# Kernel optimization log

Measured on AMD Instinct MI355X. Metric: run time of the kernel, lower is better.

The kernel has to match this reference:

```python
import jax, jax.numpy as jnp
import numpy as np
from jax import lax

B, T, H = 2, 1024, 768
E = 64          # num_experts (global pool)
I = 256         # moe_intermediate_size
TOP_K = 8       # num_experts_per_tok


def setup_inputs() -> dict:
    key = jax.random.key(0)
    k0, k1, k2, k3, k4 = jax.random.split(key, 5)
    hidden_states = jax.random.normal(k0, (B, T, H), dtype=jnp.float32)
    router_w = jax.random.normal(k1, (E, H), dtype=jnp.float32) * 0.02
    w_gate = jax.random.normal(k2, (E, H, I), dtype=jnp.float32) * 0.02
    w_up = jax.random.normal(k3, (E, H, I), dtype=jnp.float32) * 0.02
    w_down = jax.random.normal(k4, (E, I, H), dtype=jnp.float32) * 0.02
    return {"hidden_states": hidden_states, "router_w": router_w,
            "w_gate": w_gate, "w_up": w_up, "w_down": w_down}


def reference(hidden_states, router_w, w_gate, w_up, w_down):
    b, t, h = hidden_states.shape
    x = hidden_states.reshape(-1, h)                      # [N, H]
    n = x.shape[0]
    # --- Qwen3MoeTopKRouter: softmax -> top-k -> renormalize ---
    logits = x @ router_w.T                               # [N, E]
    probs = jax.nn.softmax(logits.astype(jnp.float32), axis=-1)
    top_w, top_i = lax.top_k(probs, TOP_K)                # [N, K]
    top_w = top_w / jnp.sum(top_w, axis=-1, keepdims=True)  # norm_topk_prob
    top_w = top_w.astype(x.dtype)
    # dense routing-weight matrix [N, E]; zero for unselected experts
    rw = jnp.zeros((n, E), dtype=x.dtype).at[
        jnp.arange(n)[:, None], top_i].set(top_w)
    # --- Qwen3MoeExperts: per-expert SwiGLU, combined by routing weights ---
    def step(acc, inp):
        wg, wu, wd, w = inp                               # wg/wu [H,I], wd [I,H], w [N]
        hmid = jax.nn.silu(x @ wg) * (x @ wu)             # [N, I]
        return acc + w[:, None] * (hmid @ wd), None
    out, _ = lax.scan(step, jnp.zeros_like(x),
                      (w_gate, w_up, w_down, rw.T))
    return out.reshape(b, t, h)
```

## Files before the change

kernel.cpp:

```cpp
#include <hip/hip_runtime.h>
#include <hip/hip_bf16.h>
#include <math.h>

#define N_TOK 2048
#define H_DIM 768
#define E_NUM 64
#define I_DIM 256
#define TOPK 8
#define NPAIR (N_TOK * TOPK)

typedef __attribute__((ext_vector_type(8))) short short8;
typedef __attribute__((ext_vector_type(4))) short short4v;
typedef __attribute__((ext_vector_type(4))) float f32x4;

__device__ inline ushort f2bf(float f) {
  unsigned u = __builtin_bit_cast(unsigned, f);
  u += 0x7fffu + ((u >> 16) & 1u);
  return (ushort)(u >> 16);
}

__device__ inline float bf2f(ushort h) {
  return __builtin_bit_cast(float, (unsigned)h << 16);
}

__device__ inline unsigned pack2(float a, float b) {
  return (unsigned)f2bf(a) | ((unsigned)f2bf(b) << 16);
}

__device__ inline f32x4 mfma16(short8 a, short8 b, f32x4 c) {
  return __builtin_amdgcn_mfma_f32_16x16x32_bf16(a, b, c, 0, 0, 0);
}

__device__ __forceinline__ void gload_lds16(const ushort* g, ushort* l) {
  __builtin_amdgcn_global_load_lds(
      (const __attribute__((address_space(1))) unsigned int*)g,
      (__attribute__((address_space(3))) unsigned int*)l, 16, 0, 0);
}

#define RT_KC 256
__global__ __launch_bounds__(256) void router_gemm(const float* __restrict__ x,
                                                   const float* __restrict__ rw,
                                                   float* __restrict__ part,
                                                   ushort* __restrict__ xbf) {
  const int t0 = blockIdx.x * 64, k0 = blockIdx.y * RT_KC;
  __shared__ float xs[64][68];
  __shared__ float ws[64][68];
  const int tid = threadIdx.x;
  const int tx = tid & 15, ty = tid >> 4;
  float acc[4][4] = {};
  for (int kc = 0; kc < RT_KC; kc += 64) {
    __syncthreads();
    {
      const int r = tid >> 2, q = tid & 3;
      const float4* srcx = (const float4*)&x[(size_t)(t0 + r) * H_DIM + k0 + kc];
      const float4* srcw = (const float4*)&rw[(size_t)r * H_DIM + k0 + kc];
      float4* dstx = (float4*)&xs[r][0];
      float4* dstw = (float4*)&ws[r][0];
      ushort* xb = xbf + (size_t)(t0 + r) * H_DIM + k0 + kc + q * 16;
      #pragma unroll
      for (int j = 0; j < 4; ++j) {
        float4 vx = srcx[q * 4 + j];
        dstx[q * 4 + j] = vx;
        dstw[q * 4 + j] = srcw[q * 4 + j];
        uint2 b;
        b.x = pack2(vx.x, vx.y);
        b.y = pack2(vx.z, vx.w);
        *(uint2*)(xb + j * 4) = b;
      }
    }
    __syncthreads();
    #pragma unroll
    for (int k4 = 0; k4 < 16; ++k4) {
      float4 a0 = *(float4*)&xs[ty * 4 + 0][k4 * 4];
      float4 a1 = *(float4*)&xs[ty * 4 + 1][k4 * 4];
      float4 a2 = *(float4*)&xs[ty * 4 + 2][k4 * 4];
      float4 a3 = *(float4*)&xs[ty * 4 + 3][k4 * 4];
      float4 b0 = *(float4*)&ws[tx * 4 + 0][k4 * 4];
      float4 b1 = *(float4*)&ws[tx * 4 + 1][k4 * 4];
      float4 b2 = *(float4*)&ws[tx * 4 + 2][k4 * 4];
      float4 b3 = *(float4*)&ws[tx * 4 + 3][k4 * 4];
      #define RFMA(i, j, av, bv) \
        acc[i][j] = fmaf(av.x, bv.x, fmaf(av.y, bv.y, fmaf(av.z, bv.z, fmaf(av.w, bv.w, acc[i][j]))))
      RFMA(0, 0, a0, b0); RFMA(0, 1, a0, b1); RFMA(0, 2, a0, b2); RFMA(0, 3, a0, b3);
      RFMA(1, 0, a1, b0); RFMA(1, 1, a1, b1); RFMA(1, 2, a1, b2); RFMA(1, 3, a1, b3);
      RFMA(2, 0, a2, b0); RFMA(2, 1, a2, b1); RFMA(2, 2, a2, b2); RFMA(2, 3, a2, b3);
      RFMA(3, 0, a3, b0); RFMA(3, 1, a3, b1); RFMA(3, 2, a3, b2); RFMA(3, 3, a3, b3);
      #undef RFMA
    }
  }
  float* pp = part + ((size_t)blockIdx.y * N_TOK + t0) * E_NUM;
  #pragma unroll
  for (int i = 0; i < 4; ++i)
    #pragma unroll
    for (int j = 0; j < 4; ++j)
      pp[(ty * 4 + i) * E_NUM + tx * 4 + j] = acc[i][j];
}

__global__ __launch_bounds__(256) void router_topk(const float* __restrict__ part,
                                                   int* __restrict__ topi,
                                                   float* __restrict__ topw) {
  const int t = blockIdx.x * 4 + (threadIdx.x >> 6);
  const int l = threadIdx.x & 63;
  float myv = part[(size_t)t * E_NUM + l] +
              part[((size_t)N_TOK + t) * E_NUM + l] +
              part[((size_t)2 * N_TOK + t) * E_NUM + l];
  float topv[TOPK]; int topx[TOPK];
  #pragma unroll
  for (int k = 0; k < TOPK; ++k) {
    float bv = myv; int bi = l;
    #pragma unroll
    for (int off = 32; off > 0; off >>= 1) {
      float ov = __shfl_xor(bv, off, 64);
      int oi = __shfl_xor(bi, off, 64);
      if (ov > bv || (ov == bv && oi < bi)) { bv = ov; bi = oi; }
    }
    topv[k] = bv; topx[k] = bi;
    if (l == bi) myv = -INFINITY;
  }
  if (l == 0) {
    float mx = topv[0], w[TOPK], s = 0.f;
    #pragma unroll
    for (int k = 0; k < TOPK; ++k) { w[k] = __expf(topv[k] - mx); s += w[k]; }
    float inv = 1.f / s;
    #pragma unroll
    for (int k = 0; k < TOPK; ++k) {
      topi[t * TOPK + k] = topx[k];
      topw[t * TOPK + k] = w[k] * inv;
    }
  }
}

__global__ __launch_bounds__(256) void scatter64(const int* __restrict__ topi,
                                                 int* __restrict__ offsets,
                                                 int* __restrict__ toklist,
                                                 int* __restrict__ pairpos) {
  const int e = blockIdx.x;
  const int tid = threadIdx.x, l = tid & 63, w = tid >> 6;
  __shared__ int h[E_NUM];
  __shared__ int wcnt[4];
  __shared__ int sbase;
  if (tid < E_NUM) h[tid] = 0;
  __syncthreads();
  int cnt = 0;
  for (int c = 0; c < NPAIR / 4; c += 64) {
    const int idx = w * (NPAIR / 4) + c + l;
    const int ei = topi[idx];
    atomicAdd(&h[ei], 1);
    cnt += __popcll(__ballot(ei == e));
  }
  if (l == 0) wcnt[w] = cnt;
  __syncthreads();
  if (tid == 0) {
    int s = 0;
    for (int ee = 0; ee < e; ++ee) s += h[ee];
    sbase = s;
    offsets[e] = s;
    if (e == E_NUM - 1) offsets[E_NUM] = s + h[e];
  }
  __syncthreads();
  int base = sbase;
  for (int ww = 0; ww < 4; ++ww)
    if (ww < w) base += wcnt[ww];
  for (int c = 0; c < NPAIR / 4; c += 64) {
    const int idx = w * (NPAIR / 4) + c + l;
    const bool p = (topi[idx] == e);
    const unsigned long long m = __ballot(p);
    if (p) {
      const int pos = base + __popcll(m & ((1ull << l) - 1ull));
      toklist[pos] = idx >> 3;
      pairpos[idx] = pos;
    }
    base += __popcll(m);
  }
}

#define K1_TB 192
#define KC1 64
#define NCH1 12
#define BS_ST 74
__global__ __launch_bounds__(512, 4) void k1_gateup(const ushort* __restrict__ xbf,
                                                    const float* __restrict__ wg,
                                                    const float* __restrict__ wu,
                                                    const int* __restrict__ offsets,
                                                    const int* __restrict__ toklist,
                                                    ushort* __restrict__ hmid) {
  const int e = blockIdx.y, ib = blockIdx.x;
  const int i0 = ib * 64;
  const int start = offsets[e], cnt = offsets[e + 1] - start;
  const int tokbase = blockIdx.z * K1_TB;
  if (tokbase >= cnt) return;
  const int cntb = min(K1_TB, cnt - tokbase);

  __shared__ __align__(16) ushort xs[2][K1_TB][64];
  __shared__ __align__(16) ushort Bs[128][BS_ST];
  __shared__ int tks[K1_TB];

  const int tid = threadIdx.x;
  if (tid < K1_TB) tks[tid] = toklist[start + tokbase + min(tid, cntb - 1)];
  __syncthreads();

  const int l = tid & 63, wid = tid >> 6;
  const int tf = wid & 3, icw = wid >> 2;
  const int la15 = l & 15;
  const int lxor = (l & 7) ^ ((l >> 3) & 7);

  const ushort* srcx0 = xbf + (size_t)tks[24 * wid + 0 + (l >> 3)] * H_DIM + lxor * 8;
  const ushort* srcx1 = xbf + (size_t)tks[24 * wid + 8 + (l >> 3)] * H_DIM + lxor * 8;
  const ushort* srcx2 = xbf + (size_t)tks[24 * wid + 16 + (l >> 3)] * H_DIM + lxor * 8;

  const int q = tid & 15, kp = tid >> 4;
  const float* wgp = wg + (size_t)e * H_DIM * I_DIM + i0 + 4 * q;
  const float* wup = wu + (size_t)e * H_DIM * I_DIM + i0 + 4 * q;

  f32x4 accg[3][2] = {};
  f32x4 accu[3][2] = {};
  const int ko = (l >> 4) * 8;

  float4 g0 = *(const float4*)(wgp + (size_t)(2 * kp) * I_DIM);
  float4 g1 = *(const float4*)(wgp + (size_t)(2 * kp + 1) * I_DIM);
  float4 u0 = *(const float4*)(wup + (size_t)(2 * kp) * I_DIM);
  float4 u1 = *(const float4*)(wup + (size_t)(2 * kp + 1) * I_DIM);
  gload_lds16(srcx0, &xs[0][24 * wid + 0][0]);
  gload_lds16(srcx1, &xs[0][24 * wid + 8][0]);
  gload_lds16(srcx2, &xs[0][24 * wid + 16][0]);

  for (int n = 0; n < NCH1; ++n) {
    const int cur = n & 1, nxt = cur ^ 1;
    *(unsigned*)&Bs[q * 4 + 0][2 * kp] = pack2(g0.x, g1.x);
    *(unsigned*)&Bs[q * 4 + 1][2 * kp] = pack2(g0.y, g1.y);
    *(unsigned*)&Bs[q * 4 + 2][2 * kp] = pack2(g0.z, g1.z);
    *(unsigned*)&Bs[q * 4 + 3][2 * kp] = pack2(g0.w, g1.w);
    *(unsigned*)&Bs[64 + q * 4 + 0][2 * kp] = pack2(u0.x, u1.x);
    *(unsigned*)&Bs[64 + q * 4 + 1][2 * kp] = pack2(u0.y, u1.y);
    *(unsigned*)&Bs[64 + q * 4 + 2][2 * kp] = pack2(u0.z, u1.z);
    *(unsigned*)&Bs[64 + q * 4 + 3][2 * kp] = pack2(u0.w, u1.w);
    if (n + 1 < NCH1) {
      const int kh = (n + 1) * KC1;
      g0 = *(const float4*)(wgp + (size_t)(kh + 2 * kp) * I_DIM);
      g1 = *(const float4*)(wgp + (size_t)(kh + 2 * kp + 1) * I_DIM);
      u0 = *(const float4*)(wup + (size_t)(kh + 2 * kp) * I_DIM);
      u1 = *(const float4*)(wup + (size_t)(kh + 2 * kp + 1) * I_DIM);
      gload_lds16(srcx0 + kh, &xs[nxt][24 * wid + 0][0]);
      gload_lds16(srcx1 + kh, &xs[nxt][24 * wid + 8][0]);
      gload_lds16(srcx2 + kh, &xs[nxt][24 * wid + 16][0]);
      asm volatile("s_waitcnt vmcnt(7) lgkmcnt(0)" ::: "memory");
      __builtin_amdgcn_sched_barrier(0);
      __builtin_amdgcn_s_barrier();
    } else {
      asm volatile("s_waitcnt vmcnt(0) lgkmcnt(0)" ::: "memory");
      __builtin_amdgcn_sched_barrier(0);
      __builtin_amdgcn_s_barrier();
    }
    #pragma unroll
    for (int ks = 0; ks < 2; ++ks) {
      const int kof = ks * 32 + ko;
      const int sg8 = ((ks * 4 + (l >> 4)) ^ (l & 7)) * 8;
      short8 bg0 = *(const short8*)&Bs[icw * 32 + la15][kof];
      short8 bg1 = *(const short8*)&Bs[icw * 32 + 16 + la15][kof];
      short8 bu0 = *(const short8*)&Bs[64 + icw * 32 + la15][kof];
      short8 bu1 = *(const short8*)&Bs[64 + icw * 32 + 16 + la15][kof];
      __builtin_amdgcn_s_setprio(1);
      #pragma unroll
      for (int rf = 0; rf < 3; ++rf) {
        short8 a = *(const short8*)&xs[cur][tf * 48 + rf * 16 + la15][sg8];
        accg[rf][0] = mfma16(a, bg0, accg[rf][0]);
        accg[rf][1] = mfma16(a, bg1, accg[rf][1]);
        accu[rf][0] = mfma16(a, bu0, accu[rf][0]);
        accu[rf][1] = mfma16(a, bu1, accu[rf][1]);
      }
      __builtin_amdgcn_s_setprio(0);
    }
    asm volatile("s_waitcnt lgkmcnt(0)" ::: "memory");
    __builtin_amdgcn_sched_barrier(0);
    __builtin_amdgcn_s_barrier();
  }

  ushort* tbuf = &xs[0][0][0];
  #pragma unroll
  for (int rf = 0; rf < 3; ++rf)
    #pragma unroll
    for (int c = 0; c < 2; ++c)
      #pragma unroll
      for (int jj = 0; jj < 4; ++jj) {
        const int row = tf * 48 + rf * 16 + (l >> 4) * 4 + jj;
        const int col = icw * 32 + c * 16 + la15;
        float g = accg[rf][c][jj];
        float hm = g / (1.f + __expf(-g)) * accu[rf][c][jj];
        tbuf[row * 72 + col] = f2bf(hm);
      }
  __syncthreads();
  #pragma unroll
  for (int p = 0; p < 2; ++p) {
    const int row = (tid >> 2) + p * 128, cs = tid & 3;
    if (row < cntb) {
      short8 v0 = *(const short8*)&tbuf[row * 72 + cs * 16];
      short8 v1 = *(const short8*)&tbuf[row * 72 + cs * 16 + 8];
      ushort* dst = hmid + (size_t)(start + tokbase + row) * I_DIM + i0 + cs * 16;
      *(short8*)dst = v0;
      *(short8*)(dst + 8) = v1;
    }
  }
}

#define K2_TB 256
#define KC2 128
#define DS_ST 138
__global__ __launch_bounds__(512) void k2_down(const ushort* __restrict__ hmid,
                                               const float* __restrict__ wd,
                                               const int* __restrict__ offsets,
                                               ushort* __restrict__ out_pairs) {
  const int e = blockIdx.y, hs = blockIdx.x;
  const int h0 = hs * 192;
  const int start = offsets[e], cnt = offsets[e + 1] - start;
  const int tokbase = blockIdx.z * K2_TB;
  if (tokbase >= cnt) return;
  const int tm = min(K2_TB, cnt - tokbase);

  __shared__ ushort Ds[192][DS_ST];

  const int tid = threadIdx.x, l = tid & 63, wid = tid >> 6;
  const int tf = wid & 3, ch = wid >> 2;
  const int la15 = l & 15;
  const int ko = (l >> 4) * 8;
  f32x4 acc[4][6] = {};

  int p[4];
  #pragma unroll
  for (int rf = 0; rf < 4; ++rf)
    p[rf] = min(start + tokbase + tf * 64 + rf * 16 + la15, NPAIR - 1);

  const float* wde = wd + (size_t)e * I_DIM * H_DIM;

  for (int kh = 0; kh < I_DIM; kh += KC2) {
    __syncthreads();
    #pragma unroll
    for (int it = 0; it < 6; ++it) {
      int idx = tid + it * 512;
      int qq = idx % 48, m = idx / 48;
      const int k0 = 2 * m;
      const float* src = wde + (size_t)(kh + k0) * H_DIM + h0 + qq * 4;
      float4 v0 = *(const float4*)src;
      float4 v1 = *(const float4*)(src + H_DIM);
      *(unsigned*)&Ds[qq * 4 + 0][k0] = pack2(v0.x, v1.x);
      *(unsigned*)&Ds[qq * 4 + 1][k0] = pack2(v0.y, v1.y);
      *(unsigned*)&Ds[qq * 4 + 2][k0] = pack2(v0.z, v1.z);
      *(unsigned*)&Ds[qq * 4 + 3][k0] = pack2(v0.w, v1.w);
    }
    __syncthreads();
    #pragma unroll
    for (int ks = 0; ks < 4; ++ks) {
      const int kof = ks * 32 + ko;
      short8 a[4];
      #pragma unroll
      for (int rf = 0; rf < 4; ++rf)
        a[rf] = *(const short8*)(hmid + (size_t)p[rf] * I_DIM + kh + kof);
      __builtin_amdgcn_s_setprio(1);
      #pragma unroll
      for (int cf = 0; cf < 6; ++cf) {
        short8 b = *(const short8*)&Ds[ch * 96 + cf * 16 + la15][kof];
        #pragma unroll
        for (int rf = 0; rf < 4; ++rf)
          acc[rf][cf] = mfma16(a[rf], b, acc[rf][cf]);
      }
      __builtin_amdgcn_s_setprio(0);
    }
  }

  const int rgrp = l >> 4;
  #pragma unroll
  for (int rf = 0; rf < 4; ++rf)
    #pragma unroll
    for (int jj = 0; jj < 4; ++jj) {
      int r = tf * 64 + rf * 16 + rgrp * 4 + jj;
      if (r < tm) {
        const size_t prow = (size_t)(start + tokbase + r);
        #pragma unroll
        for (int cf = 0; cf < 6; ++cf) {
          int hcol = h0 + ch * 96 + cf * 16 + la15;
          out_pairs[prow * H_DIM + hcol] = f2bf(acc[rf][cf][jj]);
        }
      }
    }
}

__global__ __launch_bounds__(192) void moe_reduce(const ushort* __restrict__ out_pairs,
                                                  const int* __restrict__ pairpos,
                                                  const float* __restrict__ topw,
                                                  float* __restrict__ out) {
  const int t = blockIdx.x;
  const int c = threadIdx.x;
  float4 acc = make_float4(0.f, 0.f, 0.f, 0.f);
  #pragma unroll
  for (int k = 0; k < TOPK; ++k) {
    const int pos = pairpos[t * TOPK + k];
    const float w = topw[t * TOPK + k];
    short4v v = *(const short4v*)&out_pairs[(size_t)pos * H_DIM + c * 4];
    acc.x = fmaf(w, bf2f((ushort)v[0]), acc.x);
    acc.y = fmaf(w, bf2f((ushort)v[1]), acc.y);
    acc.z = fmaf(w, bf2f((ushort)v[2]), acc.z);
    acc.w = fmaf(w, bf2f((ushort)v[3]), acc.w);
  }
  *(float4*)&out[(size_t)t * H_DIM + c * 4] = acc;
}

extern "C" void kernel_launch(void* const* d_in, const int* in_sizes, int n_in,
                              void* d_out, int out_size, void* d_ws, size_t ws_size,
                              hipStream_t stream) {
  const float* x  = (const float*)d_in[0];
  const float* rw = (const float*)d_in[1];
  const float* wg = (const float*)d_in[2];
  const float* wu = (const float*)d_in[3];
  const float* wd = (const float*)d_in[4];
  float* out = (float*)d_out;

  char* ws = (char*)d_ws;
  int*    topi     = (int*)(ws + 0);
  float*  topw     = (float*)(ws + 65536);
  int*    offsets  = (int*)(ws + 131072);
  int*    toklist  = (int*)(ws + 132608);
  int*    pairpos  = (int*)(ws + 264192);
  ushort* xbf      = (ushort*)(ws + 331776);
  ushort* hmid     = (ushort*)(ws + 3477504);
  float*  rpart    = (float*)(ws + 3477504);
  ushort* out_pairs= (ushort*)(ws + 11866112);

  router_gemm<<<dim3(N_TOK / 64, 3), 256, 0, stream>>>(x, rw, rpart, xbf);
  router_topk<<<N_TOK / 4, 256, 0, stream>>>(rpart, topi, topw);
  scatter64<<<E_NUM, 256, 0, stream>>>(topi, offsets, toklist, pairpos);
  k1_gateup<<<dim3(4, E_NUM, 11), 512, 0, stream>>>(xbf, wg, wu, offsets, toklist, hmid);
  k2_down<<<dim3(4, E_NUM, 8), 512, 0, stream>>>(hmid, wd, offsets, out_pairs);
  moe_reduce<<<N_TOK, 192, 0, stream>>>(out_pairs, pairpos, topw, out);
}
```

Baseline: 127.3 us.

## Fuse router GEMM and top-k selection into a single kernel

Merges the split-K router GEMM and the separate top-k kernel into one kernel. Each block computes full-K logits for 64 tokens, stages them in shared memory, and runs wave-level top-k with renormalised softmax weights. This removes a kernel launch and the global partial-logit round trip. It reduces the grid from 96 to 32 blocks and serialises the full 768-deep reduction per block, which lowers parallelism.

```diff
diff --git a/kernel.cpp b/kernel.cpp
--- a/kernel.cpp
+++ b/kernel.cpp
@@ -37,26 +37,26 @@
       (__attribute__((address_space(3))) unsigned int*)l, 16, 0, 0);
 }
 
-#define RT_KC 256
-__global__ __launch_bounds__(256) void router_gemm(const float* __restrict__ x,
-                                                   const float* __restrict__ rw,
-                                                   float* __restrict__ part,
-                                                   ushort* __restrict__ xbf) {
-  const int t0 = blockIdx.x * 64, k0 = blockIdx.y * RT_KC;
+__global__ __launch_bounds__(256) void router_fused(const float* __restrict__ x,
+                                                    const float* __restrict__ rw,
+                                                    int* __restrict__ topi,
+                                                    float* __restrict__ topw,
+                                                    ushort* __restrict__ xbf) {
+  const int t0 = blockIdx.x * 64;
   __shared__ float xs[64][68];
   __shared__ float ws[64][68];
   const int tid = threadIdx.x;
   const int tx = tid & 15, ty = tid >> 4;
   float acc[4][4] = {};
-  for (int kc = 0; kc < RT_KC; kc += 64) {
+  for (int kc = 0; kc < H_DIM; kc += 64) {
     __syncthreads();
     {
       const int r = tid >> 2, q = tid & 3;
-      const float4* srcx = (const float4*)&x[(size_t)(t0 + r) * H_DIM + k0 + kc];
-      const float4* srcw = (const float4*)&rw[(size_t)r * H_DIM + k0 + kc];
+      const float4* srcx = (const float4*)&x[(size_t)(t0 + r) * H_DIM + kc];
+      const float4* srcw = (const float4*)&rw[(size_t)r * H_DIM + kc];
       float4* dstx = (float4*)&xs[r][0];
       float4* dstw = (float4*)&ws[r][0];
-      ushort* xb = xbf + (size_t)(t0 + r) * H_DIM + k0 + kc + q * 16;
+      ushort* xb = xbf + (size_t)(t0 + r) * H_DIM + kc + q * 16;
       #pragma unroll
       for (int j = 0; j < 4; ++j) {
         float4 vx = srcx[q * 4 + j];
@@ -88,44 +88,40 @@
       #undef RFMA
     }
   }
-  float* pp = part + ((size_t)blockIdx.y * N_TOK + t0) * E_NUM;
+  __syncthreads();
   #pragma unroll
   for (int i = 0; i < 4; ++i)
     #pragma unroll
     for (int j = 0; j < 4; ++j)
-      pp[(ty * 4 + i) * E_NUM + tx * 4 + j] = acc[i][j];
-}
-
-__global__ __launch_bounds__(256) void router_topk(const float* __restrict__ part,
-                                                   int* __restrict__ topi,
-                                                   float* __restrict__ topw) {
-  const int t = blockIdx.x * 4 + (threadIdx.x >> 6);
-  const int l = threadIdx.x & 63;
-  float myv = part[(size_t)t * E_NUM + l] +
-              part[((size_t)N_TOK + t) * E_NUM + l] +
-              part[((size_t)2 * N_TOK + t) * E_NUM + l];
-  float topv[TOPK]; int topx[TOPK];
-  #pragma unroll
-  for (int k = 0; k < TOPK; ++k) {
-    float bv = myv; int bi = l;
-    #pragma unroll
-    for (int off = 32; off > 0; off >>= 1) {
-      float ov = __shfl_xor(bv, off, 64);
-      int oi = __shfl_xor(bi, off, 64);
-      if (ov > bv || (ov == bv && oi < bi)) { bv = ov; bi = oi; }
-    }
-    topv[k] = bv; topx[k] = bi;
-    if (l == bi) myv = -INFINITY;
-  }
-  if (l == 0) {
-    float mx = topv[0], w[TOPK], s = 0.f;
-    #pragma unroll
-    for (int k = 0; k < TOPK; ++k) { w[k] = __expf(topv[k] - mx); s += w[k]; }
-    float inv = 1.f / s;
+      ws[ty * 4 + i][tx * 4 + j] = acc[i][j];
+  __syncthreads();
+  const int l = tid & 63, w = tid >> 6;
+  for (int s = 0; s < 16; ++s) {
+    const int tk = w * 16 + s;
+    float myv = ws[tk][l];
+    float topv[TOPK]; int topx[TOPK];
     #pragma unroll
     for (int k = 0; k < TOPK; ++k) {
-      topi[t * TOPK + k] = topx[k];
-      topw[t * TOPK + k] = w[k] * inv;
+      float bv = myv; int bi = l;
+      #pragma unroll
+      for (int off = 32; off > 0; off >>= 1) {
+        float ov = __shfl_xor(bv, off, 64);
+        int oi = __shfl_xor(bi, off, 64);
+        if (ov > bv || (ov == bv && oi < bi)) { bv = ov; bi = oi; }
+      }
+      topv[k] = bv; topx[k] = bi;
+      if (l == bi) myv = -INFINITY;
+    }
+    if (l == 0) {
+      float mx = topv[0], wk[TOPK], sm = 0.f;
+      #pragma unroll
+      for (int k = 0; k < TOPK; ++k) { wk[k] = __expf(topv[k] - mx); sm += wk[k]; }
+      float inv = 1.f / sm;
+      #pragma unroll
+      for (int k = 0; k < TOPK; ++k) {
+        topi[(t0 + tk) * TOPK + k] = topx[k];
+        topw[(t0 + tk) * TOPK + k] = wk[k] * inv;
+      }
     }
   }
 }
@@ -421,11 +417,9 @@
   int*    pairpos  = (int*)(ws + 264192);
   ushort* xbf      = (ushort*)(ws + 331776);
   ushort* hmid     = (ushort*)(ws + 3477504);
-  float*  rpart    = (float*)(ws + 3477504);
   ushort* out_pairs= (ushort*)(ws + 11866112);
 
-  router_gemm<<<dim3(N_TOK / 64, 3), 256, 0, stream>>>(x, rw, rpart, xbf);
-  router_topk<<<N_TOK / 4, 256, 0, stream>>>(rpart, topi, topw);
+  router_fused<<<N_TOK / 64, 256, 0, stream>>>(x, rw, topi, topw, xbf);
   scatter64<<<E_NUM, 256, 0, stream>>>(topi, offsets, toklist, pairpos);
   k1_gateup<<<dim3(4, E_NUM, 11), 512, 0, stream>>>(xbf, wg, wu, offsets, toklist, hmid);
   k2_down<<<dim3(4, E_NUM, 8), 512, 0, stream>>>(hmid, wd, offsets, out_pairs);
```

Measured after the change: 214.4 us. 68.5% more time.
